# Optimization experiments

Hardware: AMD Instinct MI355X
Metric: run time of the kernel (lower is better)

## Reference

```python
import jax, jax.numpy as jnp
import numpy as np

NX = 2048
NY = 2048
LENGTH_X = 0.1
NU = 0.05
H_STEP = LENGTH_X / (NX - 1)

# 3x3 valid-conv stencils expressed as slices (identical math to conv2d cross-correlation)
def Dx(a):   return 0.5 * (a[..., 1:-1, 2:] - a[..., 1:-1, :-2])
def Dy(a):   return 0.5 * (a[..., 2:, 1:-1] - a[..., :-2, 1:-1])
def FDx(a):  return a[..., 1:-1, 2:] - a[..., 1:-1, 1:-1]
def BDx(a):  return a[..., 1:-1, 1:-1] - a[..., 1:-1, :-2]
def FDy(a):  return a[..., :-2, 1:-1] - a[..., 1:-1, 1:-1]
def BDy(a):  return a[..., 1:-1, 1:-1] - a[..., 2:, 1:-1]
def laplace(a):
    return (a[..., :-2, 1:-1] + a[..., 2:, 1:-1] + a[..., 1:-1, :-2]
            + a[..., 1:-1, 2:] - 4.0 * a[..., 1:-1, 1:-1])


def setup_inputs() -> dict:
    key = jax.random.key(0)
    k1, k2 = jax.random.split(key)
    layout = jax.random.randint(k1, (1, 2, NY, NX), 0, 12, dtype=jnp.int32)
    flow = jax.random.normal(k2, (1, 3, NY, NX), dtype=jnp.float32)
    return {"layout": layout, "flow": flow}


def _nse_core(layout, flow):
    lay = layout[0, 1]                      # [H, W] layout codes
    dt = flow.dtype
    h = jnp.asarray(H_STEP, dt)
    nu = jnp.asarray(NU, dt)

    # --- Dirichlet BC masks (scatter -> vectorized masks) ---
    ns = (lay == 2)                          # non-slip: zero all 3 channels
    G_bc = jnp.ones_like(flow) * (1.0 - ns.astype(dt))[None, None]
    G_bc_value = jnp.zeros_like(flow)

    row_in = jnp.any(lay == 1, axis=1)       # rows containing inflow
    G_bc_value = G_bc_value.at[:, 0, :, 0].set(
        jnp.where(row_in, jnp.asarray(3.0, dt), G_bc_value[:, 0, :, 0]))
    G_bc = G_bc.at[:, 0, :, 0].set(jnp.where(row_in, 0.0, G_bc[:, 0, :, 0]))
    G_bc = G_bc.at[:, 1, :, 0].set(jnp.where(row_in, 0.0, G_bc[:, 1, :, 0]))

    row_out = jnp.any(lay == 3, axis=1)      # rows containing outlet
    G_bc = G_bc.at[:, 2, :, -1].set(jnp.where(row_out, 0.0, G_bc[:, 2, :, -1]))

    x = flow * G_bc + G_bc_value             # [1,3,H,W]
    u, v, p = x[:, 0], x[:, 1], x[:, 2]      # [1,H,W]
    u_int = u[..., 1:-1, 1:-1]
    v_int = v[..., 1:-1, 1:-1]

    # Pre-compute shared stencils (each case reuses them)
    dxu, dyu = Dx(u), Dy(u)
    dxv, dyv = Dx(v), Dy(v)
    lap_u, lap_v = laplace(u), laplace(v)
    cont = dxu / h + dyv / h                 # continuity, case-independent

    def nse(case):
        if case in (4, 8, 11):
            dpx = FDx(p)
        elif case in (6, 9, 10):
            dpx = BDx(p)
        else:
            dpx = Dx(p)
        if case in (7, 10, 11):
            dpy = FDy(p)
        elif case in (5, 8, 9):
            dpy = BDy(p)
        else:
            dpy = Dy(p)
        mu = u_int * dxu / h + v_int * dyu / h + dpx / h - nu * lap_u / (h * h)
        mv = u_int * dxv / h + v_int * dyv / h + dpy / h - nu * lap_v / (h * h)
        return jnp.stack([mu, mv, cont])     # [3,1,H-2,W-2]

    # case-0 mask: G_bc with all channels zeroed where layout > 3
    G_bc0 = G_bc * (1.0 - (lay > 3).astype(dt))[None, None]
    loss_nse = G_bc0[..., 1:-1, 1:-1] * nse(0)   # broadcast -> [3,3,H-2,W-2]

    for k in range(4, 12):
        mk = (lay == k).astype(dt)[1:-1, 1:-1]   # per-case masks are channel-uniform
        loss_nse = loss_nse + mk * nse(k)

    code = jnp.where(lay > 3, lay, 0).astype(dt)  # 4*m4 + ... + 11*m11 (disjoint)
    G_bc_mask = G_bc0 + code[None, None]
    G_bc_v = jnp.stack([G_bc, G_bc_value])        # [2,1,3,H,W]
    return loss_nse, G_bc_mask, G_bc_v


def reference(layout, flow):
    return _nse_core(layout, flow)
```

## Files before the change

kernel.cpp:

```cpp
#include <hip/hip_runtime.h>

#define NXd 2048
#define NYd 2048

__global__ __launch_bounds__(256) void row_flags_kernel(const int* __restrict__ lay,
                                                        int* __restrict__ rin,
                                                        int* __restrict__ rout) {
    const int y = blockIdx.x;
    const int* row = lay + (size_t)y * NXd;
    int fin = 0, fout = 0;
    for (int x = threadIdx.x; x < NXd; x += 256) {
        const int L = row[x];
        fin  |= (L == 1);
        fout |= (L == 3);
    }
    __shared__ int s_in, s_out;
    if (threadIdx.x == 0) { s_in = 0; s_out = 0; }
    __syncthreads();
    const unsigned long long bi = __ballot(fin);
    const unsigned long long bo = __ballot(fout);
    if ((threadIdx.x & 63) == 0) {
        if (bi) atomicOr(&s_in, 1);
        if (bo) atomicOr(&s_out, 1);
    }
    __syncthreads();
    if (threadIdx.x == 0) { rin[y] = s_in; rout[y] = s_out; }
}

__global__ __launch_bounds__(256) void nse_main_kernel(const int* __restrict__ lay,
                                                       const float* __restrict__ flow,
                                                       const int* __restrict__ rin,
                                                       const int* __restrict__ rout,
                                                       float* __restrict__ out) {
    const int x = blockIdx.x * 256 + threadIdx.x;
    const int y = blockIdx.y;
    const size_t NN = (size_t)NXd * NYd;

    const float* __restrict__ f0 = flow;
    const float* __restrict__ f1 = flow + NN;
    const float* __restrict__ f2 = flow + 2 * NN;

    const size_t idxC = (size_t)y * NXd + x;
    const int LC = lay[idxC];
    const int riny = rin[y];
    const int routy = rout[y];

    float gu = (LC == 2) ? 0.f : 1.f;
    float gv = gu, gp = gu;
    float valu = 0.f;
    if (x == 0 && riny)          { gu = 0.f; gv = 0.f; valu = 3.f; }
    if (x == NXd - 1 && routy)   { gp = 0.f; }
    const float g0   = (LC > 3) ? 0.f : 1.f;
    const float code = (LC > 3) ? (float)LC : 0.f;

    float* __restrict__ out_loss = out;
    float* __restrict__ out_mask = out + (size_t)9 * 2046 * 2046;
    float* __restrict__ out_gbcv = out_mask + 3 * NN;

    out_mask[0 * NN + idxC] = gu * g0 + code;
    out_mask[1 * NN + idxC] = gv * g0 + code;
    out_mask[2 * NN + idxC] = gp * g0 + code;
    out_gbcv[0 * NN + idxC] = gu;
    out_gbcv[1 * NN + idxC] = gv;
    out_gbcv[2 * NN + idxC] = gp;
    out_gbcv[3 * NN + idxC] = valu;
    out_gbcv[4 * NN + idxC] = 0.f;
    out_gbcv[5 * NN + idxC] = 0.f;

    if (x == 0 || x == NXd - 1 || y == 0 || y == NYd - 1) return;

    const size_t iE = idxC + 1, iW = idxC - 1, iN = idxC - NXd, iS = idxC + NXd;
    const int LE = lay[iE], LW = lay[iW], LN = lay[iN], LS = lay[iS];

    const float uC = (LC == 2) ? 0.f : f0[idxC];
    const float uE = (LE == 2) ? 0.f : f0[iE];
    float       uW = (LW == 2) ? 0.f : f0[iW];
    const float uN = (LN == 2) ? 0.f : f0[iN];
    const float uS = (LS == 2) ? 0.f : f0[iS];

    const float vC = (LC == 2) ? 0.f : f1[idxC];
    const float vE = (LE == 2) ? 0.f : f1[iE];
    float       vW = (LW == 2) ? 0.f : f1[iW];
    const float vN = (LN == 2) ? 0.f : f1[iN];
    const float vS = (LS == 2) ? 0.f : f1[iS];

    if (x == 1 && riny) { uW = 3.f; vW = 0.f; }

    const float pC = (LC == 2) ? 0.f : f2[idxC];
    float       pE = (LE == 2) ? 0.f : f2[iE];
    const float pW = (LW == 2) ? 0.f : f2[iW];
    const float pN = (LN == 2) ? 0.f : f2[iN];
    const float pS = (LS == 2) ? 0.f : f2[iS];

    if (x == NXd - 2 && routy) { pE = 0.f; }

    const float dxu = 0.5f * (uE - uW);
    const float dyu = 0.5f * (uS - uN);
    const float dxv = 0.5f * (vE - vW);
    const float dyv = 0.5f * (vS - vN);
    const float lapu = uN + uS + uW + uE - 4.f * uC;
    const float lapv = vN + vS + vW + vE - 4.f * vC;

    const float invh = (float)(2047.0 / 0.1);
    const float nuh2 = (float)(0.05 * (2047.0 / 0.1) * (2047.0 / 0.1));

    const int cs = (LC > 3) ? LC : 0;
    float dpx, dpy;
    if (cs == 4 || cs == 8 || cs == 11)       dpx = pE - pC;
    else if (cs == 6 || cs == 9 || cs == 10)  dpx = pC - pW;
    else                                      dpx = 0.5f * (pE - pW);
    if (cs == 7 || cs == 10 || cs == 11)      dpy = pN - pC;
    else if (cs == 5 || cs == 8 || cs == 9)   dpy = pC - pS;
    else                                      dpy = 0.5f * (pS - pN);

    const float zm = (LC == 2) ? 0.f : 1.f;
    const float mu   = zm * ((uC * dxu + vC * dyu + dpx) * invh - lapu * nuh2);
    const float mv   = zm * ((uC * dxv + vC * dyv + dpy) * invh - lapv * nuh2);
    const float cont = zm * ((dxu + dyv) * invh);

    const size_t PS = (size_t)2046 * 2046;
    const size_t li = (size_t)(y - 1) * 2046 + (x - 1);
    out_loss[0 * PS + li] = mu;
    out_loss[1 * PS + li] = mu;
    out_loss[2 * PS + li] = mu;
    out_loss[3 * PS + li] = mv;
    out_loss[4 * PS + li] = mv;
    out_loss[5 * PS + li] = mv;
    out_loss[6 * PS + li] = cont;
    out_loss[7 * PS + li] = cont;
    out_loss[8 * PS + li] = cont;
}

extern "C" void kernel_launch(void* const* d_in, const int* in_sizes, int n_in,
                              void* d_out, int out_size, void* d_ws, size_t ws_size,
                              hipStream_t stream) {
    const int*   layout = (const int*)d_in[0];
    const float* flow   = (const float*)d_in[1];
    const int*   lay    = layout + (size_t)NYd * NXd;
    float* out = (float*)d_out;
    int* rin  = (int*)d_ws;
    int* rout = rin + NYd;

    row_flags_kernel<<<NYd, 256, 0, stream>>>(lay, rin, rout);

    dim3 grid(NXd / 256, NYd, 1);
    nse_main_kernel<<<grid, dim3(256, 1, 1), 0, stream>>>(lay, flow, rin, rout, out);
}
```

Baseline: 408.1 us.

## Split mask and loss work into separate vectorized kernels with float4 loads

Splits the single per-pixel kernel into a mask/G_bc kernel and an interior loss kernel. The mask kernel writes its outputs as float4 vectors. The loss kernel processes four columns per thread, using float4 loads for the center, north and south rows and scalar loads for the west and east halos. The row-flag scan also reads the layout as int4. The aim is to cut memory instruction count and improve load/store width on this bandwidth-bound kernel. The trade-off is that loss stores are still scalar with a 16-byte stride between neighboring threads, which may reduce store coalescing, and the work now needs one extra kernel launch.

```diff
diff --git a/kernel.cpp b/kernel.cpp
--- a/kernel.cpp
+++ b/kernel.cpp
@@ -3,16 +3,19 @@
 #define NXd 2048
 #define NYd 2048
 
+typedef int   i4 __attribute__((ext_vector_type(4)));
+typedef float f4 __attribute__((ext_vector_type(4)));
+
 __global__ __launch_bounds__(256) void row_flags_kernel(const int* __restrict__ lay,
                                                         int* __restrict__ rin,
                                                         int* __restrict__ rout) {
     const int y = blockIdx.x;
-    const int* row = lay + (size_t)y * NXd;
+    const i4* row = (const i4*)(lay + (size_t)y * NXd);
     int fin = 0, fout = 0;
-    for (int x = threadIdx.x; x < NXd; x += 256) {
-        const int L = row[x];
-        fin  |= (L == 1);
-        fout |= (L == 3);
+    for (int x = threadIdx.x; x < NXd / 4; x += 256) {
+        const i4 L = row[x];
+        #pragma unroll
+        for (int e = 0; e < 4; ++e) { fin |= (L[e] == 1); fout |= (L[e] == 3); }
     }
     __shared__ int s_in, s_out;
     if (threadIdx.x == 0) { s_in = 0; s_out = 0; }
@@ -27,108 +30,143 @@
     if (threadIdx.x == 0) { rin[y] = s_in; rout[y] = s_out; }
 }
 
-__global__ __launch_bounds__(256) void nse_main_kernel(const int* __restrict__ lay,
-                                                       const float* __restrict__ flow,
-                                                       const int* __restrict__ rin,
-                                                       const int* __restrict__ rout,
-                                                       float* __restrict__ out) {
-    const int x = blockIdx.x * 256 + threadIdx.x;
-    const int y = blockIdx.y;
+__global__ __launch_bounds__(256) void mask_kernel(const int* __restrict__ lay,
+                                                   const int* __restrict__ rin,
+                                                   const int* __restrict__ rout,
+                                                   float* __restrict__ out) {
     const size_t NN = (size_t)NXd * NYd;
+    const int g = blockIdx.x * 256 + threadIdx.x;
+    const int x4 = (g * 4) & (NXd - 1);
+    const int y  = (g * 4) >> 11;
+    const i4 L = ((const i4*)lay)[g];
+    const int riny = rin[y], routy = rout[y];
+
+    f4 m0, m1, m2, g0v, g1v, g2v, valv, zv;
+    #pragma unroll
+    for (int e = 0; e < 4; ++e) {
+        const int Le = L[e];
+        const float gb = (Le == 2) ? 0.f : 1.f;
+        float gu = gb, gv = gb, gp = gb, valu = 0.f;
+        if (x4 == 0 && e == 0 && riny)          { gu = 0.f; gv = 0.f; valu = 3.f; }
+        if (x4 == NXd - 4 && e == 3 && routy)   { gp = 0.f; }
+        const float gz   = (Le > 3) ? 0.f : 1.f;
+        const float code = (Le > 3) ? (float)Le : 0.f;
+        m0[e] = gu * gz + code;
+        m1[e] = gv * gz + code;
+        m2[e] = gp * gz + code;
+        g0v[e] = gu; g1v[e] = gv; g2v[e] = gp;
+        valv[e] = valu; zv[e] = 0.f;
+    }
+
+    f4* out_mask = (f4*)(out + (size_t)9 * 2046 * 2046);
+    f4* out_gbcv = out_mask + 3 * (NN / 4);
+    const size_t Q = NN / 4;
+    out_mask[0 * Q + g] = m0;
+    out_mask[1 * Q + g] = m1;
+    out_mask[2 * Q + g] = m2;
+    out_gbcv[0 * Q + g] = g0v;
+    out_gbcv[1 * Q + g] = g1v;
+    out_gbcv[2 * Q + g] = g2v;
+    out_gbcv[3 * Q + g] = valv;
+    out_gbcv[4 * Q + g] = zv;
+    out_gbcv[5 * Q + g] = zv;
+}
+
+__global__ __launch_bounds__(256) void loss_kernel(const int* __restrict__ lay,
+                                                   const float* __restrict__ flow,
+                                                   const int* __restrict__ rin,
+                                                   const int* __restrict__ rout,
+                                                   float* __restrict__ out) {
+    const size_t NN = (size_t)NXd * NYd;
+    const int g = blockIdx.x * 256 + threadIdx.x;
+    const int y = blockIdx.y + 1;
+    const int x4 = g * 4;
+    const size_t rowC = (size_t)y * NXd;
+    const int gi = (int)(rowC >> 2) + g;
+    const int R = NXd / 4;
+
+    const i4 LC4 = ((const i4*)lay)[gi];
+    const i4 LN4 = ((const i4*)lay)[gi - R];
+    const i4 LS4 = ((const i4*)lay)[gi + R];
+    const int LW = (g > 0)   ? lay[rowC + x4 - 1] : 0;
+    const int LE = (g < 511) ? lay[rowC + x4 + 4] : 0;
 
     const float* __restrict__ f0 = flow;
     const float* __restrict__ f1 = flow + NN;
     const float* __restrict__ f2 = flow + 2 * NN;
 
-    const size_t idxC = (size_t)y * NXd + x;
-    const int LC = lay[idxC];
-    const int riny = rin[y];
-    const int routy = rout[y];
+    f4 uC = ((const f4*)f0)[gi], uN = ((const f4*)f0)[gi - R], uS = ((const f4*)f0)[gi + R];
+    f4 vC = ((const f4*)f1)[gi], vN = ((const f4*)f1)[gi - R], vS = ((const f4*)f1)[gi + R];
+    f4 pC = ((const f4*)f2)[gi], pN = ((const f4*)f2)[gi - R], pS = ((const f4*)f2)[gi + R];
+    float uWs = (g > 0)   ? f0[rowC + x4 - 1] : 0.f;
+    float vWs = (g > 0)   ? f1[rowC + x4 - 1] : 0.f;
+    float pWs = (g > 0)   ? f2[rowC + x4 - 1] : 0.f;
+    float uEs = (g < 511) ? f0[rowC + x4 + 4] : 0.f;
+    float vEs = (g < 511) ? f1[rowC + x4 + 4] : 0.f;
+    float pEs = (g < 511) ? f2[rowC + x4 + 4] : 0.f;
 
-    float gu = (LC == 2) ? 0.f : 1.f;
-    float gv = gu, gp = gu;
-    float valu = 0.f;
-    if (x == 0 && riny)          { gu = 0.f; gv = 0.f; valu = 3.f; }
-    if (x == NXd - 1 && routy)   { gp = 0.f; }
-    const float g0   = (LC > 3) ? 0.f : 1.f;
-    const float code = (LC > 3) ? (float)LC : 0.f;
+    #pragma unroll
+    for (int e = 0; e < 4; ++e) {
+        if (LC4[e] == 2) { uC[e] = 0.f; vC[e] = 0.f; pC[e] = 0.f; }
+        if (LN4[e] == 2) { uN[e] = 0.f; vN[e] = 0.f; pN[e] = 0.f; }
+        if (LS4[e] == 2) { uS[e] = 0.f; vS[e] = 0.f; pS[e] = 0.f; }
+    }
+    if (LW == 2) { uWs = 0.f; vWs = 0.f; pWs = 0.f; }
+    if (LE == 2) { uEs = 0.f; vEs = 0.f; pEs = 0.f; }
 
-    float* __restrict__ out_loss = out;
-    float* __restrict__ out_mask = out + (size_t)9 * 2046 * 2046;
-    float* __restrict__ out_gbcv = out_mask + 3 * NN;
+    const int riny = rin[y], routy = rout[y];
+    if (g == 0 && riny)     { uC[0] = 3.f; vC[0] = 0.f; }
+    if (g == 511 && routy)  { pC[3] = 0.f; }
 
-    out_mask[0 * NN + idxC] = gu * g0 + code;
-    out_mask[1 * NN + idxC] = gv * g0 + code;
-    out_mask[2 * NN + idxC] = gp * g0 + code;
-    out_gbcv[0 * NN + idxC] = gu;
-    out_gbcv[1 * NN + idxC] = gv;
-    out_gbcv[2 * NN + idxC] = gp;
-    out_gbcv[3 * NN + idxC] = valu;
-    out_gbcv[4 * NN + idxC] = 0.f;
-    out_gbcv[5 * NN + idxC] = 0.f;
-
-    if (x == 0 || x == NXd - 1 || y == 0 || y == NYd - 1) return;
-
-    const size_t iE = idxC + 1, iW = idxC - 1, iN = idxC - NXd, iS = idxC + NXd;
-    const int LE = lay[iE], LW = lay[iW], LN = lay[iN], LS = lay[iS];
-
-    const float uC = (LC == 2) ? 0.f : f0[idxC];
-    const float uE = (LE == 2) ? 0.f : f0[iE];
-    float       uW = (LW == 2) ? 0.f : f0[iW];
-    const float uN = (LN == 2) ? 0.f : f0[iN];
-    const float uS = (LS == 2) ? 0.f : f0[iS];
-
-    const float vC = (LC == 2) ? 0.f : f1[idxC];
-    const float vE = (LE == 2) ? 0.f : f1[iE];
-    float       vW = (LW == 2) ? 0.f : f1[iW];
-    const float vN = (LN == 2) ? 0.f : f1[iN];
-    const float vS = (LS == 2) ? 0.f : f1[iS];
-
-    if (x == 1 && riny) { uW = 3.f; vW = 0.f; }
-
-    const float pC = (LC == 2) ? 0.f : f2[idxC];
-    float       pE = (LE == 2) ? 0.f : f2[iE];
-    const float pW = (LW == 2) ? 0.f : f2[iW];
-    const float pN = (LN == 2) ? 0.f : f2[iN];
-    const float pS = (LS == 2) ? 0.f : f2[iS];
-
-    if (x == NXd - 2 && routy) { pE = 0.f; }
-
-    const float dxu = 0.5f * (uE - uW);
-    const float dyu = 0.5f * (uS - uN);
-    const float dxv = 0.5f * (vE - vW);
-    const float dyv = 0.5f * (vS - vN);
-    const float lapu = uN + uS + uW + uE - 4.f * uC;
-    const float lapv = vN + vS + vW + vE - 4.f * vC;
-
-    const float invh = (float)(2047.0 / 0.1);
-    const float nuh2 = (float)(0.05 * (2047.0 / 0.1) * (2047.0 / 0.1));
-
-    const int cs = (LC > 3) ? LC : 0;
-    float dpx, dpy;
-    if (cs == 4 || cs == 8 || cs == 11)       dpx = pE - pC;
-    else if (cs == 6 || cs == 9 || cs == 10)  dpx = pC - pW;
-    else                                      dpx = 0.5f * (pE - pW);
-    if (cs == 7 || cs == 10 || cs == 11)      dpy = pN - pC;
-    else if (cs == 5 || cs == 8 || cs == 9)   dpy = pC - pS;
-    else                                      dpy = 0.5f * (pS - pN);
-
-    const float zm = (LC == 2) ? 0.f : 1.f;
-    const float mu   = zm * ((uC * dxu + vC * dyu + dpx) * invh - lapu * nuh2);
-    const float mv   = zm * ((uC * dxv + vC * dyv + dpy) * invh - lapv * nuh2);
-    const float cont = zm * ((dxu + dyv) * invh);
+    const float invh = 20470.0f;
+    const float nuh2 = 0.05f * 20470.0f * 20470.0f;
 
     const size_t PS = (size_t)2046 * 2046;
-    const size_t li = (size_t)(y - 1) * 2046 + (x - 1);
-    out_loss[0 * PS + li] = mu;
-    out_loss[1 * PS + li] = mu;
-    out_loss[2 * PS + li] = mu;
-    out_loss[3 * PS + li] = mv;
-    out_loss[4 * PS + li] = mv;
-    out_loss[5 * PS + li] = mv;
-    out_loss[6 * PS + li] = cont;
-    out_loss[7 * PS + li] = cont;
-    out_loss[8 * PS + li] = cont;
+    float* __restrict__ out_loss = out;
+
+    #pragma unroll
+    for (int e = 0; e < 4; ++e) {
+        const int x = x4 + e;
+        if (x < 1 || x > NXd - 2) continue;
+        const float uW = (e == 0) ? uWs : uC[e - 1];
+        const float uE = (e == 3) ? uEs : uC[e + 1];
+        const float vW = (e == 0) ? vWs : vC[e - 1];
+        const float vE = (e == 3) ? vEs : vC[e + 1];
+        const float pW = (e == 0) ? pWs : pC[e - 1];
+        const float pE = (e == 3) ? pEs : pC[e + 1];
+
+        const float dxu = 0.5f * (uE - uW);
+        const float dyu = 0.5f * (uS[e] - uN[e]);
+        const float dxv = 0.5f * (vE - vW);
+        const float dyv = 0.5f * (vS[e] - vN[e]);
+        const float lapu = uN[e] + uS[e] + uW + uE - 4.f * uC[e];
+        const float lapv = vN[e] + vS[e] + vW + vE - 4.f * vC[e];
+
+        const int cs = (LC4[e] > 3) ? LC4[e] : 0;
+        float dpx, dpy;
+        if (cs == 4 || cs == 8 || cs == 11)       dpx = pE - pC[e];
+        else if (cs == 6 || cs == 9 || cs == 10)  dpx = pC[e] - pW;
+        else                                      dpx = 0.5f * (pE - pW);
+        if (cs == 7 || cs == 10 || cs == 11)      dpy = pN[e] - pC[e];
+        else if (cs == 5 || cs == 8 || cs == 9)   dpy = pC[e] - pS[e];
+        else                                      dpy = 0.5f * (pS[e] - pN[e]);
+
+        const float zm = (LC4[e] == 2) ? 0.f : 1.f;
+        const float mu   = zm * ((uC[e] * dxu + vC[e] * dyu + dpx) * invh - lapu * nuh2);
+        const float mv   = zm * ((uC[e] * dxv + vC[e] * dyv + dpy) * invh - lapv * nuh2);
+        const float cont = zm * ((dxu + dyv) * invh);
+
+        const size_t li = (size_t)(y - 1) * 2046 + (x - 1);
+        out_loss[0 * PS + li] = mu;
+        out_loss[1 * PS + li] = mu;
+        out_loss[2 * PS + li] = mu;
+        out_loss[3 * PS + li] = mv;
+        out_loss[4 * PS + li] = mv;
+        out_loss[5 * PS + li] = mv;
+        out_loss[6 * PS + li] = cont;
+        out_loss[7 * PS + li] = cont;
+        out_loss[8 * PS + li] = cont;
+    }
 }
 
 extern "C" void kernel_launch(void* const* d_in, const int* in_sizes, int n_in,
@@ -143,6 +181,9 @@
 
     row_flags_kernel<<<NYd, 256, 0, stream>>>(lay, rin, rout);
 
-    dim3 grid(NXd / 256, NYd, 1);
-    nse_main_kernel<<<grid, dim3(256, 1, 1), 0, stream>>>(lay, flow, rin, rout, out);
+    const size_t NN = (size_t)NXd * NYd;
+    mask_kernel<<<(int)(NN / 4 / 256), 256, 0, stream>>>(lay, rin, rout, out);
+
+    dim3 grid(2, NYd - 2, 1);
+    loss_kernel<<<grid, dim3(256, 1, 1), 0, stream>>>(lay, flow, rin, rout, out);
 }
```

New measurement: 472.1 us. 1.16x slower.
